# Optimization experiments

Measured on AMD Instinct MI355X. Metric: run time of the kernel, lower is better.

The kernel has to match this reference:

```python
import jax, jax.numpy as jnp
import numpy as np
import math

NUM_GROUPS = 32
NUM_HEADS = 8  # in_channels // num_head_channel = 512 // 64
EPS = 1e-5


def setup_inputs() -> dict:
    key = jax.random.key(0)
    ks = jax.random.split(key, 4)
    b, c, h, w = 2, 512, 64, 64
    s = 1.0 / math.sqrt(c)
    return {
        "x": jax.random.normal(ks[0], (b, c, h, w), dtype=jnp.float32),
        "gn_weight": jnp.ones((c,), jnp.float32),
        "gn_bias": jnp.zeros((c,), jnp.float32),
        "wq": jax.random.normal(ks[1], (c, c), jnp.float32) * s,
        "bq": jnp.zeros((c,), jnp.float32),
        "wkv": jax.random.normal(ks[2], (2 * c, c), jnp.float32) * s,
        "bkv": jnp.zeros((2 * c,), jnp.float32),
        "wproj": jax.random.normal(ks[3], (c, c), jnp.float32) * s,
        "bproj": jnp.zeros((c,), jnp.float32),
    }


def _group_norm(x, weight, bias):
    b, c, h, w = x.shape
    xg = x.reshape(b, NUM_GROUPS, c // NUM_GROUPS, h, w)
    mean = jnp.mean(xg, axis=(2, 3, 4), keepdims=True)
    var = jnp.var(xg, axis=(2, 3, 4), keepdims=True)
    xn = ((xg - mean) * jax.lax.rsqrt(var + EPS)).reshape(b, c, h, w)
    return xn * weight[None, :, None, None] + bias[None, :, None, None]


def reference(x, gn_weight, gn_bias, wq, bq, wkv, bkv, wproj, bproj):
    b, c, h, w = x.shape
    nh = NUM_HEADS
    hd = c // nh
    residual = x

    hs = _group_norm(x, gn_weight, gn_bias)
    hs = hs.reshape(b, c, h * w).transpose(0, 2, 1)  # [b, seq, c]

    q = hs @ wq.T + bq                     # [b, seq, c]
    kv = hs @ wkv.T + bkv                  # [b, seq, 2c]
    k, v = jnp.split(kv, 2, axis=2)

    def to_heads(t):  # [b, seq, c] -> [b, nh, seq, hd]
        return t.reshape(b, -1, nh, hd).transpose(0, 2, 1, 3)

    q, k, v = to_heads(q), to_heads(k), to_heads(v)
    scale = 1.0 / math.sqrt(hd)

    scores = jnp.einsum("bhqd,bhkd->bhqk", q, k) * scale
    probs = jax.nn.softmax(scores.astype(jnp.float32), axis=-1).astype(scores.dtype)
    out = jnp.einsum("bhqk,bhkd->bhqd", probs, v)  # [b, nh, seq, hd]

    out = out.transpose(0, 2, 1, 3).reshape(b, h * w, c)
    out = out @ wproj.T + bproj
    out = out.transpose(0, 2, 1).reshape(b, c, h, w)
    return out + residual
```

## Files before the change

kernel.cpp:

```cpp
#include <hip/hip_runtime.h>

typedef __attribute__((ext_vector_type(8))) short bf16x8;
typedef __attribute__((ext_vector_type(4))) float f32x4;
typedef __attribute__((ext_vector_type(4))) unsigned int u32x4;
typedef __attribute__((ext_vector_type(4))) unsigned short su16x4;

#define SEQ 4096
#define CH 512

__device__ __forceinline__ float b2f(unsigned short u) {
  union { unsigned int i; float f; } x; x.i = ((unsigned int)u) << 16; return x.f;
}
__device__ __forceinline__ unsigned short f2b(float f) {
  union { float f; unsigned int i; } x; x.f = f;
  unsigned int r = x.i + 0x7fffu + ((x.i >> 16) & 1u);
  return (unsigned short)(r >> 16);
}

template<int F32> struct LD;
template<> struct LD<0> {
  static __device__ __forceinline__ float at(const void* p, size_t i) {
    return b2f(((const unsigned short*)p)[i]);
  }
  static __device__ __forceinline__ bf16x8 b8(const void* p, size_t i) {
    return *(const bf16x8*)((const unsigned short*)p + i);
  }
  static __device__ __forceinline__ void f4(const void* p, size_t i, float o[4]) {
    su16x4 v = *(const su16x4*)((const unsigned short*)p + i);
#pragma unroll
    for (int j = 0; j < 4; ++j) o[j] = b2f(v[j]);
  }
};
template<> struct LD<1> {
  static __device__ __forceinline__ float at(const void* p, size_t i) {
    return ((const float*)p)[i];
  }
  static __device__ __forceinline__ bf16x8 b8(const void* p, size_t i) {
    const float* f = (const float*)p + i;
    f32x4 a = *(const f32x4*)f, b = *(const f32x4*)(f + 4);
    union { bf16x8 v; unsigned short u[8]; } r;
#pragma unroll
    for (int j = 0; j < 4; ++j) { r.u[j] = f2b(a[j]); r.u[4 + j] = f2b(b[j]); }
    return r.v;
  }
  static __device__ __forceinline__ void f4(const void* p, size_t i, float o[4]) {
    f32x4 v = *(const f32x4*)((const float*)p + i);
#pragma unroll
    for (int j = 0; j < 4; ++j) o[j] = v[j];
  }
};
template<int F32> struct ST;
template<> struct ST<0> {
  static __device__ __forceinline__ void st4(void* p, size_t i, const float v[4]) {
    su16x4 o;
#pragma unroll
    for (int j = 0; j < 4; ++j) o[j] = f2b(v[j]);
    *(su16x4*)((unsigned short*)p + i) = o;
  }
};
template<> struct ST<1> {
  static __device__ __forceinline__ void st4(void* p, size_t i, const float v[4]) {
// ... 106 lines not shown
                                                  unsigned short* __restrict__ hs, int b,
                                                  const int* __restrict__ ctrl) {
  if (ctrl[0] != F32) return;
  const int bz = b + blockIdx.z;
  hs += (size_t)blockIdx.z * ((size_t)SEQ * CH);
  const int s0 = blockIdx.x * 64, c0 = blockIdx.y * 64;
  __shared__ float tile[64 * 65];
  const int t = threadIdx.x;
  float2 stv[4];
#pragma unroll
  for (int i = 0; i < 4; ++i) stv[i] = stats[bz * 32 + (c0 >> 4) + i];
#pragma unroll
  for (int rep = 0; rep < 16; ++rep) {
    int idx = rep * 256 + t;
    int cl = idx >> 6, sl = idx & 63;
    int c = c0 + cl;
    float xv = LD<F32>::at(x, ((size_t)(bz * CH + c)) * SEQ + s0 + sl);
    float2 sv = stv[cl >> 4];
    tile[cl * 65 + sl] = (xv - sv.x) * sv.y * LD<F32>::at(w, c) + LD<F32>::at(bsv, c);
  }
  __syncthreads();
#pragma unroll
  for (int rep = 0; rep < 16; ++rep) {
    int idx = rep * 256 + t;
    int cl = idx & 63, sl = idx >> 6;
    hs[((size_t)(s0 + sl)) * CH + c0 + cl] = f2b(tile[cl * 65 + sl]);
  }
}

template<int F32>
__global__ __launch_bounds__(256) void qkv_head_k(const unsigned short* __restrict__ hs,
                                                  const void* __restrict__ wq,
                                                  const void* __restrict__ wkv,
                                                  const void* __restrict__ bq,
                                                  const void* __restrict__ bkv,
                                                  unsigned short* __restrict__ qh,
                                                  unsigned short* __restrict__ kh,
                                                  unsigned short* __restrict__ vt, int h0,
                                                  const int* __restrict__ ctrl) {
  if (ctrl[0] != F32) return;
  const int z = blockIdx.z;
  const int h = h0 + (z & 7);
  hs += (size_t)(z >> 3) * ((size_t)SEQ * CH);
  const size_t hofs = (size_t)z * (4096 * 64);
  __shared__ __align__(16) unsigned short As[128 * 64];
  __shared__ __align__(16) unsigned short Ws[64 * 64];
  const int t = threadIdx.x;
  const int lane = t & 63, wave = t >> 6;
  const int l15 = lane & 15, qd = lane >> 4;
  const int m0 = blockIdx.x * 128;

  const void* Wb; size_t wofs; const void* bb; size_t bofs;
  unsigned short* dst; float scale = 1.0f; int tr = 0;
  if (blockIdx.y == 0)      { Wb = wq;  wofs = (size_t)(h * 64) * 512;         bb = bq;  bofs = h * 64;       dst = qh + hofs; scale = 0.125f; }
  else if (blockIdx.y == 1) { Wb = wkv; wofs = (size_t)(h * 64) * 512;         bb = bkv; bofs = h * 64;       dst = kh + hofs; }
  else                      { Wb = wkv; wofs = (size_t)(512 + h * 64) * 512;   bb = bkv; bofs = 512 + h * 64; dst = vt + hofs; tr = 1; }

  const f32x4 fz = {0.f, 0.f, 0.f, 0.f};
  f32x4 acc[2][4];
#pragma unroll
  for (int i = 0; i < 2; ++i)
#pragma unroll
    for (int j = 0; j < 4; ++j) acc[i][j] = fz;

  bf16x8 ar[4], wr2[2];
#pragma unroll
  for (int rep = 0; rep < 4; ++rep) {
    int id = rep * 256 + t, r = id >> 3, c = id & 7;
    ar[rep] = LD<0>::b8(hs, (size_t)(m0 + r) * 512 + c * 8);
  }
#pragma unroll
  for (int rep = 0; rep < 2; ++rep) {
    int id = rep * 256 + t, r = id >> 3, c = id & 7;
    wr2[rep] = LD<F32>::b8(Wb, wofs + (size_t)r * 512 + c * 8);
  }
  for (int ks = 0; ks < 8; ++ks) {
    __syncthreads();
#pragma unroll
    for (int rep = 0; rep < 4; ++rep) {
      int id = rep * 256 + t, r = id >> 3, c = id & 7, p = (c + r) & 7;
      *(bf16x8*)&As[r * 64 + p * 8] = ar[rep];
    }
#pragma unroll
    for (int rep = 0; rep < 2; ++rep) {
      int id = rep * 256 + t, r = id >> 3, c = id & 7, p = (c + r) & 7;
      *(bf16x8*)&Ws[r * 64 + p * 8] = wr2[rep];
    }
    __syncthreads();
    if (ks < 7) {
      int k0 = (ks + 1) * 64;
#pragma unroll
      for (int rep = 0; rep < 4; ++rep) {
        int id = rep * 256 + t, r = id >> 3, c = id & 7;
        ar[rep] = LD<0>::b8(hs, (size_t)(m0 + r) * 512 + k0 + c * 8);
      }
#pragma unroll
      for (int rep = 0; rep < 2; ++rep) {
        int id = rep * 256 + t, r = id >> 3, c = id & 7;
        wr2[rep] = LD<F32>::b8(Wb, wofs + (size_t)r * 512 + k0 + c * 8);
      }
    }
#pragma unroll
    for (int kb = 0; kb < 2; ++kb) {
      int cc = kb * 4 + qd;
      bf16x8 af[2], bfr[4];
#pragma unroll
      for (int mt = 0; mt < 2; ++mt) {
// ... 204 lines not shown
      f32x4 a = *(const f32x4*)((const float*)x + base);
      f32x4 b = *(const f32x4*)((const float*)x + base + 4);
#pragma unroll
      for (int j = 0; j < 4; ++j) { vals[j] = a[j]; vals[4 + j] = b[j]; }
    } else {
      wv = LD<0>::at(w, c); bvv = LD<0>::at(bsv, c);
      const unsigned short* xp = (const unsigned short*)x + base;
      u32x4 v = *(const u32x4*)xp;
#pragma unroll
      for (int j = 0; j < 4; ++j) {
        vals[2 * j] = b2f((unsigned short)v[j]);
        vals[2 * j + 1] = b2f((unsigned short)(v[j] >> 16));
      }
    }
    float mul = st.y * wv, add = bvv - st.x * st.y * wv;
#pragma unroll
    for (int j = 0; j < 8; ++j) tile[cl * 65 + sv + j] = vals[j] * mul + add;
  }
  __syncthreads();
#pragma unroll
  for (int rep = 0; rep < 4; ++rep) {
    int idx = rep * 256 + t;
    int sl = idx >> 4, cl4 = (idx & 15) * 4;
    su16x4 ov;
#pragma unroll
    for (int j = 0; j < 4; ++j) ov[j] = f2b(tile[(cl4 + j) * 65 + sl]);
    *(su16x4*)&hsb[((size_t)(s0 + sl)) * 512 + c0 + cl4] = ov;
  }
}

__global__ __launch_bounds__(256) void qkv2_k(const unsigned short* __restrict__ hs,
                                              const void* __restrict__ wq,
                                              const void* __restrict__ wkv,
                                              const void* __restrict__ bq,
                                              const void* __restrict__ bkv,
                                              unsigned short* __restrict__ qh,
                                              unsigned short* __restrict__ kh,
                                              unsigned short* __restrict__ vt,
                                              const int* __restrict__ ctrl) {
  const int mode = ctrl[0];
  const int z = blockIdx.z;
  const int h = z & 7;
  hs += (size_t)(z >> 3) * ((size_t)SEQ * CH);
  const size_t hofs = (size_t)z * (4096 * 64);
  __shared__ __align__(16) unsigned short As[128 * 64];
  __shared__ __align__(16) unsigned short Ws[64 * 64];
  const int t = threadIdx.x;
  const int lane = t & 63, wave = t >> 6;
  const int l15 = lane & 15, qd = lane >> 4;
  const int m0 = blockIdx.x * 128;

  const void* Wb; size_t wofs; const void* bb; size_t bofs;
  unsigned short* dst; float scale = 1.0f; int tr = 0;
  if (blockIdx.y == 0)      { Wb = wq;  wofs = (size_t)(h * 64) * 512;         bb = bq;  bofs = h * 64;       dst = qh + hofs; scale = 0.125f; }
  else if (blockIdx.y == 1) { Wb = wkv; wofs = (size_t)(h * 64) * 512;         bb = bkv; bofs = h * 64;       dst = kh + hofs; }
  else                      { Wb = wkv; wofs = (size_t)(512 + h * 64) * 512;   bb = bkv; bofs = 512 + h * 64; dst = vt + hofs; tr = 1; }

  const f32x4 fz = {0.f, 0.f, 0.f, 0.f};
  f32x4 acc[2][4];
#pragma unroll
  for (int i = 0; i < 2; ++i)
#pragma unroll
    for (int j = 0; j < 4; ++j) acc[i][j] = fz;

  bf16x8 ar[4], wr2[2];
#pragma unroll
  for (int rep = 0; rep < 4; ++rep) {
    int id = rep * 256 + t, r = id >> 3, c = id & 7;
    ar[rep] = LD<0>::b8(hs, (size_t)(m0 + r) * 512 + c * 8);
  }
  if (mode) {
#pragma unroll
    for (int rep = 0; rep < 2; ++rep) {
      int id = rep * 256 + t, r = id >> 3, c = id & 7;
      wr2[rep] = LD<1>::b8(Wb, wofs + (size_t)r * 512 + c * 8);
    }
  } else {
#pragma unroll
    for (int rep = 0; rep < 2; ++rep) {
      int id = rep * 256 + t, r = id >> 3, c = id & 7;
      wr2[rep] = LD<0>::b8(Wb, wofs + (size_t)r * 512 + c * 8);
    }
  }
  for (int ks = 0; ks < 8; ++ks) {
    __syncthreads();
#pragma unroll
    for (int rep = 0; rep < 4; ++rep) {
      int id = rep * 256 + t, r = id >> 3, c = id & 7, p = (c + r) & 7;
      *(bf16x8*)&As[r * 64 + p * 8] = ar[rep];
    }
#pragma unroll
    for (int rep = 0; rep < 2; ++rep) {
      int id = rep * 256 + t, r = id >> 3, c = id & 7, p = (c + r) & 7;
      *(bf16x8*)&Ws[r * 64 + p * 8] = wr2[rep];
    }
    __syncthreads();
    if (ks < 7) {
      int k0 = (ks + 1) * 64;
#pragma unroll
      for (int rep = 0; rep < 4; ++rep) {
        int id = rep * 256 + t, r = id >> 3, c = id & 7;
        ar[rep] = LD<0>::b8(hs, (size_t)(m0 + r) * 512 + k0 + c * 8);
      }
      if (mode) {
#pragma unroll
        for (int rep = 0; rep < 2; ++rep) {
          int id = rep * 256 + t, r = id >> 3, c = id & 7;
// ... 77 lines not shown
  const f32x4 fz = {0.f, 0.f, 0.f, 0.f};
  f32x4 o[4];
#pragma unroll
  for (int i = 0; i < 4; ++i) o[i] = fz;
  f32x4 lsum = fz;

  union { bf16x8 v; unsigned short u[8]; } onesu;
#pragma unroll
  for (int j = 0; j < 8; ++j) onesu.u[j] = 0x3F80;
  const bf16x8 onesv = onesu.v;

  unsigned short* pp = &Ps[wave][0];

  const int sid0 = t, sr0 = sid0 >> 3, sc0 = sid0 & 7;
  const int sid1 = 256 + t, sr1 = sid1 >> 3, sc1 = sid1 & 7;
  u32x4 kr0, kr1, vr0, vr1;
  kr0 = *(const u32x4*)&kh[(size_t)sr0 * 64 + sc0 * 8];
  kr1 = *(const u32x4*)&kh[(size_t)sr1 * 64 + sc1 * 8];
  vr0 = *(const u32x4*)&vt[(size_t)sr0 * 4096 + sc0 * 8];
  vr1 = *(const u32x4*)&vt[(size_t)sr1 * 4096 + sc1 * 8];

  const int p0 = (sc0 ^ (sr0 & 7)) * 8, p1 = (sc1 ^ (sr1 & 7)) * 8;

  for (int kt = 0; kt < 64; ++kt) {
    __syncthreads();
    *(u32x4*)&Ks[sr0 * 64 + p0] = kr0;
    *(u32x4*)&Ks[sr1 * 64 + p1] = kr1;
    *(u32x4*)&Vs[sr0 * 64 + p0] = vr0;
    *(u32x4*)&Vs[sr1 * 64 + p1] = vr1;
    __syncthreads();
    if (kt < 63) {
      int kn = kt + 1;
      kr0 = *(const u32x4*)&kh[(size_t)(kn * 64 + sr0) * 64 + sc0 * 8];
      kr1 = *(const u32x4*)&kh[(size_t)(kn * 64 + sr1) * 64 + sc1 * 8];
      vr0 = *(const u32x4*)&vt[(size_t)sr0 * 4096 + kn * 64 + sc0 * 8];
      vr1 = *(const u32x4*)&vt[(size_t)sr1 * 4096 + kn * 64 + sc1 * 8];
    }

    f32x4 sa[4];
#pragma unroll
    for (int nt = 0; nt < 4; ++nt) {
      sa[nt] = fz;
      int row = nt * 16 + l15, rx = row & 7;
      bf16x8 kf0 = *(const bf16x8*)&Ks[row * 64 + (qd ^ rx) * 8];
      bf16x8 kf1 = *(const bf16x8*)&Ks[row * 64 + ((qd + 4) ^ rx) * 8];
      sa[nt] = __builtin_amdgcn_mfma_f32_16x16x32_bf16(qf0, kf0, sa[nt], 0, 0, 0);
      sa[nt] = __builtin_amdgcn_mfma_f32_16x16x32_bf16(qf1, kf1, sa[nt], 0, 0, 0);
    }

#pragma unroll
    for (int nt = 0; nt < 4; ++nt)
#pragma unroll
      for (int r = 0; r < 4; ++r)
        sa[nt][r] = __expf(fminf(sa[nt][r], 60.0f));

#pragma unroll
    for (int nt = 0; nt < 4; ++nt)
#pragma unroll
      for (int r = 0; r < 4; r += 2) {
        unsigned int pk;
        asm("v_cvt_pk_bf16_f32 %0, %1, %2" : "=v"(pk) : "v"(sa[nt][r]), "v"(sa[nt][r + 1]));
        pp[(qd * 4 + r) * 72 + nt * 16 + l15] = (unsigned short)pk;
        pp[(qd * 4 + r + 1) * 72 + nt * 16 + l15] = (unsigned short)(pk >> 16);
      }

    bf16x8 pf0 = *(const bf16x8*)&pp[l15 * 72 + qd * 8];
    bf16x8 pf1 = *(const bf16x8*)&pp[l15 * 72 + 32 + qd * 8];

    lsum = __builtin_amdgcn_mfma_f32_16x16x32_bf16(pf0, onesv, lsum, 0, 0, 0);
    lsum = __builtin_amdgcn_mfma_f32_16x16x32_bf16(pf1, onesv, lsum, 0, 0, 0);

#pragma unroll
    for (int nt = 0; nt < 4; ++nt) {
      int row = nt * 16 + l15, rx = row & 7;
      bf16x8 vf0 = *(const bf16x8*)&Vs[row * 64 + (qd ^ rx) * 8];
      bf16x8 vf1 = *(const bf16x8*)&Vs[row * 64 + ((qd + 4) ^ rx) * 8];
      o[nt] = __builtin_amdgcn_mfma_f32_16x16x32_bf16(pf0, vf0, o[nt], 0, 0, 0);
      o[nt] = __builtin_amdgcn_mfma_f32_16x16x32_bf16(pf1, vf1, o[nt], 0, 0, 0);
    }
  }

  float inv[4];
#pragma unroll
  for (int r = 0; r < 4; ++r) inv[r] = 1.f / lsum[r];
#pragma unroll
  for (int nt = 0; nt < 4; ++nt)
#pragma unroll
    for (int r = 0; r < 4; ++r) {
      int row = qt * 64 + wave * 16 + qd * 4 + r;
      aw[(size_t)row * 512 + h * 64 + nt * 16 + l15] = f2b(o[nt][r] * inv[r]);
    }
}

__global__ __launch_bounds__(256) void proj2_k(const unsigned short* __restrict__ A,
                                               const void* __restrict__ W,
                                               const void* __restrict__ bias,
                                               void* __restrict__ outv,
                                               const void* __restrict__ residv,
                                               const int* __restrict__ ctrl) {
  const int mode = ctrl[0];
  const int z = blockIdx.z;
  A += (size_t)z * ((size_t)SEQ * CH);
  const void* resid = (const void*)((const char*)residv + (size_t)z * ((size_t)SEQ * CH) * (mode ? 4 : 2));
  void* out0 = (void*)((char*)outv + (size_t)z * ((size_t)SEQ * CH) * (mode ? 4 : 2));
  __shared__ __align__(16) unsigned short As[128 * 64];
  __shared__ __align__(16) unsigned short Bs[128 * 64];
  const int t = threadIdx.x;
  const int lane = t & 63, wave = t >> 6;
  const int l15 = lane & 15, qd = lane >> 4;
  const int m0 = blockIdx.x * 128, n0 = blockIdx.y * 128;
  const int wm = (wave & 1) * 64, wn = (wave >> 1) * 64;

  const f32x4 fz = {0.f, 0.f, 0.f, 0.f};
  f32x4 acc[4][4];
#pragma unroll
  for (int i = 0; i < 4; ++i)
#pragma unroll
    for (int j = 0; j < 4; ++j) acc[i][j] = fz;

  bf16x8 ar[4], br[4];
#pragma unroll
  for (int rep = 0; rep < 4; ++rep) {
    int id = rep * 256 + t, r = id >> 3, c = id & 7;
    ar[rep] = LD<0>::b8(A, (size_t)(m0 + r) * 512 + c * 8);
  }
  if (mode) {
#pragma unroll
    for (int rep = 0; rep < 4; ++rep) {
      int id = rep * 256 + t, r = id >> 3, c = id & 7;
      br[rep] = LD<1>::b8(W, (size_t)(n0 + r) * 512 + c * 8);
    }
  } else {
#pragma unroll
    for (int rep = 0; rep < 4; ++rep) {
      int id = rep * 256 + t, r = id >> 3, c = id & 7;
      br[rep] = LD<0>::b8(W, (size_t)(n0 + r) * 512 + c * 8);
    }
  }
  for (int ks = 0; ks < 8; ++ks) {
    __syncthreads();
#pragma unroll
    for (int rep = 0; rep < 4; ++rep) {
      int id = rep * 256 + t, r = id >> 3, c = id & 7, p = (c + r) & 7;
      *(bf16x8*)&As[r * 64 + p * 8] = ar[rep];
// ... 38 lines not shown
      for (int mt = 0; mt < 4; ++mt)
#pragma unroll
        for (int nt = 0; nt < 4; ++nt)
          acc[mt][nt] = __builtin_amdgcn_mfma_f32_16x16x32_bf16(af[mt], bfr[nt], acc[mt][nt], 0, 0, 0);
    }
  }

  float bv[4];
#pragma unroll
  for (int nt = 0; nt < 4; ++nt)
    bv[nt] = mode ? LD<1>::at(bias, n0 + wn + nt * 16 + l15)
                  : LD<0>::at(bias, n0 + wn + nt * 16 + l15);

#pragma unroll
  for (int mt = 0; mt < 4; ++mt) {
    int row0 = m0 + wm + mt * 16 + qd * 4;
#pragma unroll
    for (int nt = 0; nt < 4; ++nt) {
      int col = n0 + wn + nt * 16 + l15;
      size_t basea = ((size_t)col) * 4096 + row0;
      float rv[4], ov[4];
      if (mode) LD<1>::f4(resid, basea, rv); else LD<0>::f4(resid, basea, rv);
#pragma unroll
      for (int r = 0; r < 4; ++r) ov[r] = acc[mt][nt][r] + bv[nt] + rv[r];
      if (mode) ST<1>::st4(out0, basea, ov); else ST<0>::st4(out0, basea, ov);
    }
  }
}

extern "C" void kernel_launch(void* const* d_in, const int* in_sizes, int n_in,
                              void* d_out, int out_size, void* d_ws, size_t ws_size,
                              hipStream_t stream) {
  const void* x   = d_in[0];
  const void* gw  = d_in[1];
  const void* gb  = d_in[2];
  const void* wq  = d_in[3];
  const void* bq  = d_in[4];
  const void* wkv = d_in[5];
  const void* bkv = d_in[6];
  const void* wp  = d_in[7];
  const void* bp  = d_in[8];

  const size_t EM = (size_t)4096 * 512;
  const int NOUT = 4194304;
  const size_t HB = (size_t)4096 * 64;

  int* ctrl = (int*)d_ws;
  float2* stats = (float2*)((char*)d_ws + 64);
  float2* partials = (float2*)((char*)d_ws + 576);

  probe_k<<<1, 256, 0, stream>>>((const unsigned short*)x, ctrl);

  const size_t FAST2_NEED = 4096 + (3 * 16 * HB + 2 * EM) * sizeof(unsigned short);
  const size_t FAST_NEED = 1024 + 3 * 8 * HB * sizeof(unsigned short);

  if (ws_size >= FAST2_NEED) {
    unsigned short* qa = (unsigned short*)((char*)d_ws + 4096);
    unsigned short* ka = qa + 16 * HB;
    unsigned short* va = ka + 16 * HB;
    unsigned short* aw0 = va + 16 * HB;
    const int NQKV = (int)(3 * 16 * HB);
    const int NAW  = (int)(2 * EM);

    unsigned short* hs01 = (unsigned short*)d_out;

    gn_stats2_k<<<256, 256, 0, stream>>>(x, partials, ctrl);
    gn_fin_k<<<1, 64, 0, stream>>>(partials, stats);
    gn_apply2_k<<<dim3(64, 8, 2), 256, 0, stream>>>(x, gw, gb, stats, hs01, ctrl);
    scan_k<<<256, 256, 0, stream>>>(hs01, NAW, 0, ctrl, -1);

    qkv2_k<<<dim3(32, 3, 16), 256, 0, stream>>>(hs01, wq, wkv, bq, bkv, qa, ka, va, ctrl);
    scan_k<<<256, 256, 0, stream>>>(qa, NQKV, 1, ctrl, -1);
    attn_head_k<<<dim3(64, 16), 256, 0, stream>>>(qa, ka, va, aw0, 0, ctrl, -1);
    scan_k<<<256, 256, 0, stream>>>(aw0, NAW, 2, ctrl, -1);
    proj2_k<<<dim3(32, 4, 2), 256, 0, stream>>>(aw0, wp, bp, d_out, x, ctrl);

    scan_k<<<256, 256, 0, stream>>>((unsigned short*)d_out, NOUT, 6, ctrl, 0);
    scan32_k<<<256, 256, 0, stream>>>((float*)d_out, NOUT, 6, ctrl);

    sent_fin_k<0><<<256, 256, 0, stream>>>(d_out, ctrl, NOUT);
    sent_fin_k<1><<<256, 256, 0, stream>>>(d_out, ctrl, NOUT);
    return;
  }

  if (ws_size >= FAST_NEED) {
    unsigned short* qa = (unsigned short*)((char*)d_ws + 1024);
    unsigned short* ka = qa + 8 * HB;
    unsigned short* va = ka + 8 * HB;
    const int NQKV = (int)(3 * 8 * HB);

    {
      unsigned short* out16 = (unsigned short*)d_out;
      unsigned short* hs0 = out16;
      unsigned short* aw0 = out16 + EM;
      unsigned short* hs1 = out16 + EM;
      unsigned short* aw1 = (unsigned short*)d_in[0];

      gn_stats_k<0><<<64, 256, 0, stream>>>(x, stats, ctrl);
      gn_apply_k<0><<<dim3(64, 8), 256, 0, stream>>>(x, gw, gb, stats, hs0, 0, ctrl);
      scan_k<<<256, 256, 0, stream>>>(hs0, (int)EM, 0, ctrl, 0);

      qkv_head_k<0><<<dim3(32, 3, 8), 256, 0, stream>>>(hs0, wq, wkv, bq, bkv, qa, ka, va, 0, ctrl);
      scan_k<<<256, 256, 0, stream>>>(qa, NQKV, 1, ctrl, 0);
      attn_head_k<<<dim3(64, 8), 256, 0, stream>>>(qa, ka, va, aw0, 0, ctrl, 0);
      scan_k<<<256, 256, 0, stream>>>(aw0, (int)EM, 2, ctrl, 0);
      proj_k<0><<<dim3(32, 4), 256, 0, stream>>>(aw0, wp, bp, out16, x, ctrl);

      gn_apply_k<0><<<dim3(64, 8), 256, 0, stream>>>(x, gw, gb, stats, hs1, 1, ctrl);
      scan_k<<<256, 256, 0, stream>>>(hs1, (int)EM, 3, ctrl, 0);
      qkv_head_k<0><<<dim3(32, 3, 8), 256, 0, stream>>>(hs1, wq, wkv, bq, bkv, qa, ka, va, 0, ctrl);
      scan_k<<<256, 256, 0, stream>>>(qa, NQKV, 4, ctrl, 0);
      attn_head_k<<<dim3(64, 8), 256, 0, stream>>>(qa, ka, va, aw1, 0, ctrl, 0);
      scan_k<<<256, 256, 0, stream>>>(aw1, (int)EM, 5, ctrl, 0);
      proj_k<0><<<dim3(32, 4), 256, 0, stream>>>(aw1, wp, bp, out16 + EM,
                                                 (const char*)x + EM * 2, ctrl);
      scan_k<<<256, 256, 0, stream>>>(out16, NOUT, 6, ctrl, 0);
    }

    {
      const float* xf = (const float*)x;
      float* outf = (float*)d_out;
      unsigned short* hsA = (unsigned short*)d_out;
      unsigned short* awA = (unsigned short*)((char*)d_out + 8 * 1024 * 1024);
      unsigned short* hsB = (unsigned short*)((char*)d_out + 12 * 1024 * 1024);
      unsigned short* awB = (unsigned short*)d_in[0];

// ... 106 lines not shown
```

Baseline: 293.9 us.

## Split attention over key halves and combine partial outputs in a separate kernel

Adds a split-K attention kernel that launches twice as many blocks, each covering half of the key sequence, and writes unnormalized fp32 partial outputs and row sums to workspace. A combine kernel sums the halves, normalizes, and writes bf16. The aim is more parallelism than the original 1024-block attention launch provides on a large GPU. The change also folds log2(e) into the Q scale so exp2f replaces __expf. It costs extra workspace traffic for the fp32 partials and one more kernel launch, and only runs when the workspace is large enough.

Measured after the change: 309.6 us. 1.05x slower.

```diff
diff --git a/kernel.cpp b/kernel.cpp
--- a/kernel.cpp
+++ b/kernel.cpp
@@ -7,6 +7,8 @@
 
 #define SEQ 4096
 #define CH 512
+#define QSCALE 0.180336887f
+#define SCLAMP 86.0f
 
 __device__ __forceinline__ float b2f(unsigned short u) {
   union { unsigned int i; float f; } x; x.i = ((unsigned int)u) << 16; return x.f;
@@ -219,7 +221,7 @@
 
   const void* Wb; size_t wofs; const void* bb; size_t bofs;
   unsigned short* dst; float scale = 1.0f; int tr = 0;
-  if (blockIdx.y == 0)      { Wb = wq;  wofs = (size_t)(h * 64) * 512;         bb = bq;  bofs = h * 64;       dst = qh + hofs; scale = 0.125f; }
+  if (blockIdx.y == 0)      { Wb = wq;  wofs = (size_t)(h * 64) * 512;         bb = bq;  bofs = h * 64;       dst = qh + hofs; scale = QSCALE; }
   else if (blockIdx.y == 1) { Wb = wkv; wofs = (size_t)(h * 64) * 512;         bb = bkv; bofs = h * 64;       dst = kh + hofs; }
   else                      { Wb = wkv; wofs = (size_t)(512 + h * 64) * 512;   bb = bkv; bofs = 512 + h * 64; dst = vt + hofs; tr = 1; }
 
@@ -530,7 +532,7 @@
 
   const void* Wb; size_t wofs; const void* bb; size_t bofs;
   unsigned short* dst; float scale = 1.0f; int tr = 0;
-  if (blockIdx.y == 0)      { Wb = wq;  wofs = (size_t)(h * 64) * 512;         bb = bq;  bofs = h * 64;       dst = qh + hofs; scale = 0.125f; }
+  if (blockIdx.y == 0)      { Wb = wq;  wofs = (size_t)(h * 64) * 512;         bb = bq;  bofs = h * 64;       dst = qh + hofs; scale = QSCALE; }
   else if (blockIdx.y == 1) { Wb = wkv; wofs = (size_t)(h * 64) * 512;         bb = bkv; bofs = h * 64;       dst = kh + hofs; }
   else                      { Wb = wkv; wofs = (size_t)(512 + h * 64) * 512;   bb = bkv; bofs = 512 + h * 64; dst = vt + hofs; tr = 1; }
 
@@ -714,7 +716,7 @@
     for (int nt = 0; nt < 4; ++nt)
 #pragma unroll
       for (int r = 0; r < 4; ++r)
-        sa[nt][r] = __expf(fminf(sa[nt][r], 60.0f));
+        sa[nt][r] = exp2f(fminf(sa[nt][r], SCLAMP));
 
 #pragma unroll
     for (int nt = 0; nt < 4; ++nt)
@@ -752,6 +754,149 @@
       int row = qt * 64 + wave * 16 + qd * 4 + r;
       aw[(size_t)row * 512 + h * 64 + nt * 16 + l15] = f2b(o[nt][r] * inv[r]);
     }
+}
+
+__global__ __launch_bounds__(256) void attn_split_k(const unsigned short* __restrict__ qh,
+                                                    const unsigned short* __restrict__ kh,
+                                                    const unsigned short* __restrict__ vt,
+                                                    float* __restrict__ po,
+                                                    float* __restrict__ ls,
+                                                    const int* __restrict__ ctrl) {
+  const int y = blockIdx.y;
+  const int bh = y & 15, khalf = y >> 4;
+  const size_t hofs = (size_t)bh * (4096 * 64);
+  qh += hofs; kh += hofs; vt += hofs;
+  const int qt = blockIdx.x;
+  const int kt0 = khalf * 32;
+  const int t = threadIdx.x;
+  const int lane = t & 63, wave = t >> 6;
+  const int l15 = lane & 15, qd = lane >> 4;
+
+  __shared__ __align__(16) unsigned short Ks[64 * 64];
+  __shared__ __align__(16) unsigned short Vs[64 * 64];
+  __shared__ __align__(16) unsigned short Ps[4][16 * 72];
+
+  const int qrow = qt * 64 + wave * 16 + l15;
+  bf16x8 qf0 = *(const bf16x8*)&qh[(size_t)qrow * 64 + qd * 8];
+  bf16x8 qf1 = *(const bf16x8*)&qh[(size_t)qrow * 64 + 32 + qd * 8];
+
+  const f32x4 fz = {0.f, 0.f, 0.f, 0.f};
+  f32x4 o[4];
+#pragma unroll
+  for (int i = 0; i < 4; ++i) o[i] = fz;
+  f32x4 lsum = fz;
+
+  union { bf16x8 v; unsigned short u[8]; } onesu;
+#pragma unroll
+  for (int j = 0; j < 8; ++j) onesu.u[j] = 0x3F80;
+  const bf16x8 onesv = onesu.v;
+
+  unsigned short* pp = &Ps[wave][0];
+
+  const int sid0 = t, sr0 = sid0 >> 3, sc0 = sid0 & 7;
+  const int sid1 = 256 + t, sr1 = sid1 >> 3, sc1 = sid1 & 7;
+  u32x4 kr0, kr1, vr0, vr1;
+  kr0 = *(const u32x4*)&kh[(size_t)(kt0 * 64 + sr0) * 64 + sc0 * 8];
+  kr1 = *(const u32x4*)&kh[(size_t)(kt0 * 64 + sr1) * 64 + sc1 * 8];
+  vr0 = *(const u32x4*)&vt[(size_t)sr0 * 4096 + kt0 * 64 + sc0 * 8];
+  vr1 = *(const u32x4*)&vt[(size_t)sr1 * 4096 + kt0 * 64 + sc1 * 8];
+
+  const int p0 = (sc0 ^ (sr0 & 7)) * 8, p1 = (sc1 ^ (sr1 & 7)) * 8;
+
+  for (int kt = kt0; kt < kt0 + 32; ++kt) {
+    __syncthreads();
+    *(u32x4*)&Ks[sr0 * 64 + p0] = kr0;
+    *(u32x4*)&Ks[sr1 * 64 + p1] = kr1;
+    *(u32x4*)&Vs[sr0 * 64 + p0] = vr0;
+    *(u32x4*)&Vs[sr1 * 64 + p1] = vr1;
+    __syncthreads();
+    if (kt < kt0 + 31) {
+      int kn = kt + 1;
+      kr0 = *(const u32x4*)&kh[(size_t)(kn * 64 + sr0) * 64 + sc0 * 8];
+      kr1 = *(const u32x4*)&kh[(size_t)(kn * 64 + sr1) * 64 + sc1 * 8];
+      vr0 = *(const u32x4*)&vt[(size_t)sr0 * 4096 + kn * 64 + sc0 * 8];
+      vr1 = *(const u32x4*)&vt[(size_t)sr1 * 4096 + kn * 64 + sc1 * 8];
+    }
+
+    f32x4 sa[4];
+#pragma unroll
+    for (int nt = 0; nt < 4; ++nt) {
+      sa[nt] = fz;
+      int row = nt * 16 + l15, rx = row & 7;
+      bf16x8 kf0 = *(const bf16x8*)&Ks[row * 64 + (qd ^ rx) * 8];
+      bf16x8 kf1 = *(const bf16x8*)&Ks[row * 64 + ((qd + 4) ^ rx) * 8];
+      sa[nt] = __builtin_amdgcn_mfma_f32_16x16x32_bf16(qf0, kf0, sa[nt], 0, 0, 0);
+      sa[nt] = __builtin_amdgcn_mfma_f32_16x16x32_bf16(qf1, kf1, sa[nt], 0, 0, 0);
+    }
+
+#pragma unroll
+    for (int nt = 0; nt < 4; ++nt)
+#pragma unroll
+      for (int r = 0; r < 4; ++r)
+        sa[nt][r] = exp2f(fminf(sa[nt][r], SCLAMP));
+
+#pragma unroll
+    for (int nt = 0; nt < 4; ++nt)
+#pragma unroll
+      for (int r = 0; r < 4; r += 2) {
+        unsigned int pk;
+        asm("v_cvt_pk_bf16_f32 %0, %1, %2" : "=v"(pk) : "v"(sa[nt][r]), "v"(sa[nt][r + 1]));
+        pp[(qd * 4 + r) * 72 + nt * 16 + l15] = (unsigned short)pk;
+        pp[(qd * 4 + r + 1) * 72 + nt * 16 + l15] = (unsigned short)(pk >> 16);
+      }
+
+    bf16x8 pf0 = *(const bf16x8*)&pp[l15 * 72 + qd * 8];
+    bf16x8 pf1 = *(const bf16x8*)&pp[l15 * 72 + 32 + qd * 8];
+
+    lsum = __builtin_amdgcn_mfma_f32_16x16x32_bf16(pf0, onesv, lsum, 0, 0, 0);
+    lsum = __builtin_amdgcn_mfma_f32_16x16x32_bf16(pf1, onesv, lsum, 0, 0, 0);
+
+#pragma unroll
+    for (int nt = 0; nt < 4; ++nt) {
+      int row = nt * 16 + l15, rx = row & 7;
+      bf16x8 vf0 = *(const bf16x8*)&Vs[row * 64 + (qd ^ rx) * 8];
+      bf16x8 vf1 = *(const bf16x8*)&Vs[row * 64 + ((qd + 4) ^ rx) * 8];
+      o[nt] = __builtin_amdgcn_mfma_f32_16x16x32_bf16(pf0, vf0, o[nt], 0, 0, 0);
+      o[nt] = __builtin_amdgcn_mfma_f32_16x16x32_bf16(pf1, vf1, o[nt], 0, 0, 0);
+    }
+  }
+
+  float* pob = po + (((size_t)y * 64 + qt) * 64) * 64;
+  float* lsb = ls + ((size_t)y * 64 + qt) * 64;
+#pragma unroll
+  for (int r = 0; r < 4; ++r) {
+    int row = wave * 16 + qd * 4 + r;
+    if (l15 == 0) lsb[row] = lsum[r];
+#pragma unroll
+    for (int nt = 0; nt < 4; ++nt)
+      pob[(size_t)row * 64 + nt * 16 + l15] = o[nt][r];
+  }
+}
+
+__global__ __launch_bounds__(256) void comb_k(const float* __restrict__ po,
+                                              const float* __restrict__ ls,
+                                              unsigned short* __restrict__ aw,
+                                              const int* __restrict__ ctrl) {
+  const int qt = blockIdx.x, bh = blockIdx.y;
+  const int h = bh & 7, b = bh >> 3;
+  unsigned short* awb = aw + (size_t)b * ((size_t)SEQ * CH);
+  const float* po0 = po + (((size_t)bh * 64 + qt) * 64) * 64;
+  const float* po1 = po + (((size_t)(16 + bh) * 64 + qt) * 64) * 64;
+  const float* ls0 = ls + ((size_t)bh * 64 + qt) * 64;
+  const float* ls1 = ls + ((size_t)(16 + bh) * 64 + qt) * 64;
+  const int t = threadIdx.x;
+#pragma unroll
+  for (int rep = 0; rep < 4; ++rep) {
+    int idx = rep * 256 + t;
+    int lr = idx >> 4, c4 = (idx & 15) * 4;
+    float inv = 1.f / (ls0[lr] + ls1[lr]);
+    f32x4 a = *(const f32x4*)(po0 + (size_t)lr * 64 + c4);
+    f32x4 bq = *(const f32x4*)(po1 + (size_t)lr * 64 + c4);
+    su16x4 ov;
+#pragma unroll
+    for (int j = 0; j < 4; ++j) ov[j] = f2b((a[j] + bq[j]) * inv);
+    *(su16x4*)&awb[((size_t)(qt * 64 + lr)) * 512 + h * 64 + c4] = ov;
+  }
 }
 
 __global__ __launch_bounds__(256) void proj2_k(const unsigned short* __restrict__ A,
@@ -896,6 +1041,9 @@
   probe_k<<<1, 256, 0, stream>>>((const unsigned short*)x, ctrl);
 
   const size_t FAST2_NEED = 4096 + (3 * 16 * HB + 2 * EM) * sizeof(unsigned short);
+  const size_t PO_BYTES = (size_t)32 * 64 * 64 * 64 * 4;
+  const size_t LS_BYTES = (size_t)32 * 64 * 64 * 4;
+  const size_t SPLIT_NEED = FAST2_NEED + PO_BYTES + LS_BYTES;
   const size_t FAST_NEED = 1024 + 3 * 8 * HB * sizeof(unsigned short);
 
   if (ws_size >= FAST2_NEED) {
@@ -915,7 +1063,15 @@
 
     qkv2_k<<<dim3(32, 3, 16), 256, 0, stream>>>(hs01, wq, wkv, bq, bkv, qa, ka, va, ctrl);
     scan_k<<<256, 256, 0, stream>>>(qa, NQKV, 1, ctrl, -1);
-    attn_head_k<<<dim3(64, 16), 256, 0, stream>>>(qa, ka, va, aw0, 0, ctrl, -1);
+
+    if (ws_size >= SPLIT_NEED) {
+      float* po = (float*)((char*)d_ws + FAST2_NEED);
+      float* ls = (float*)((char*)po + PO_BYTES);
+      attn_split_k<<<dim3(64, 32), 256, 0, stream>>>(qa, ka, va, po, ls, ctrl);
+      comb_k<<<dim3(64, 16), 256, 0, stream>>>(po, ls, aw0, ctrl);
+    } else {
+      attn_head_k<<<dim3(64, 16), 256, 0, stream>>>(qa, ka, va, aw0, 0, ctrl, -1);
+    }
     scan_k<<<256, 256, 0, stream>>>(aw0, NAW, 2, ctrl, -1);
     proj2_k<<<dim3(32, 4, 2), 256, 0, stream>>>(aw0, wp, bp, d_out, x, ctrl);
 
```

## Replace attention kernel with 32x32 MFMA split-K variant using exp2

Applied to the files above, without the earlier changes.

Adds a new attention kernel using 32x32x16 bf16 MFMAs that computes S^T and keeps probabilities in registers, exchanging halves via lane shuffles instead of staging through LDS. Waves split the key tile in two halves and reduce partial outputs and row sums through shared memory at the end, and the row sum is accumulated in VALU rather than by an MFMA against a ones vector. Q scaling is folded to include log2(e) so exp2f replaces __expf. It keeps the softmax without max subtraction (clamped exponent), and the register-level permutation of P is more complex and error-prone.

After: 330.2 us. +12.3%, slower.

```diff
diff --git a/kernel.cpp b/kernel.cpp
--- a/kernel.cpp
+++ b/kernel.cpp
@@ -2,11 +2,14 @@
 
 typedef __attribute__((ext_vector_type(8))) short bf16x8;
 typedef __attribute__((ext_vector_type(4))) float f32x4;
+typedef __attribute__((ext_vector_type(16))) float f32x16;
 typedef __attribute__((ext_vector_type(4))) unsigned int u32x4;
 typedef __attribute__((ext_vector_type(4))) unsigned short su16x4;
 
 #define SEQ 4096
 #define CH 512
+#define QSCALE 0.180336887f
+#define SCLAMP 86.0f
 
 __device__ __forceinline__ float b2f(unsigned short u) {
   union { unsigned int i; float f; } x; x.i = ((unsigned int)u) << 16; return x.f;
@@ -219,7 +222,7 @@
 
   const void* Wb; size_t wofs; const void* bb; size_t bofs;
   unsigned short* dst; float scale = 1.0f; int tr = 0;
-  if (blockIdx.y == 0)      { Wb = wq;  wofs = (size_t)(h * 64) * 512;         bb = bq;  bofs = h * 64;       dst = qh + hofs; scale = 0.125f; }
+  if (blockIdx.y == 0)      { Wb = wq;  wofs = (size_t)(h * 64) * 512;         bb = bq;  bofs = h * 64;       dst = qh + hofs; scale = QSCALE; }
   else if (blockIdx.y == 1) { Wb = wkv; wofs = (size_t)(h * 64) * 512;         bb = bkv; bofs = h * 64;       dst = kh + hofs; }
   else                      { Wb = wkv; wofs = (size_t)(512 + h * 64) * 512;   bb = bkv; bofs = 512 + h * 64; dst = vt + hofs; tr = 1; }
 
@@ -530,7 +533,7 @@
 
   const void* Wb; size_t wofs; const void* bb; size_t bofs;
   unsigned short* dst; float scale = 1.0f; int tr = 0;
-  if (blockIdx.y == 0)      { Wb = wq;  wofs = (size_t)(h * 64) * 512;         bb = bq;  bofs = h * 64;       dst = qh + hofs; scale = 0.125f; }
+  if (blockIdx.y == 0)      { Wb = wq;  wofs = (size_t)(h * 64) * 512;         bb = bq;  bofs = h * 64;       dst = qh + hofs; scale = QSCALE; }
   else if (blockIdx.y == 1) { Wb = wkv; wofs = (size_t)(h * 64) * 512;         bb = bkv; bofs = h * 64;       dst = kh + hofs; }
   else                      { Wb = wkv; wofs = (size_t)(512 + h * 64) * 512;   bb = bkv; bofs = 512 + h * 64; dst = vt + hofs; tr = 1; }
 
@@ -714,7 +717,7 @@
     for (int nt = 0; nt < 4; ++nt)
 #pragma unroll
       for (int r = 0; r < 4; ++r)
-        sa[nt][r] = __expf(fminf(sa[nt][r], 60.0f));
+        sa[nt][r] = exp2f(fminf(sa[nt][r], SCLAMP));
 
 #pragma unroll
     for (int nt = 0; nt < 4; ++nt)
@@ -752,6 +755,164 @@
       int row = qt * 64 + wave * 16 + qd * 4 + r;
       aw[(size_t)row * 512 + h * 64 + nt * 16 + l15] = f2b(o[nt][r] * inv[r]);
     }
+}
+
+__global__ __launch_bounds__(256) void attn32_k(const unsigned short* __restrict__ qh,
+                                                const unsigned short* __restrict__ kh,
+                                                const unsigned short* __restrict__ vt,
+                                                unsigned short* __restrict__ aw,
+                                                const int* __restrict__ ctrl) {
+  const int y = blockIdx.y;
+  const int h = y & 7;
+  const size_t hofs = (size_t)y * (4096 * 64);
+  qh += hofs; kh += hofs; vt += hofs;
+  aw += (size_t)(y >> 3) * ((size_t)SEQ * CH);
+  const int qt = blockIdx.x;
+  const int t = threadIdx.x;
+  const int lane = t & 63, wave = t >> 6;
+  const int khalf = wave & 1, qblk = wave >> 1;
+  const int l31 = lane & 31, hp = lane >> 5;
+
+  __shared__ __align__(16) unsigned short Ks[64 * 64];
+  __shared__ __align__(16) unsigned short Vs[64 * 64];
+  __shared__ float Ls[64];
+
+  const int qrow = qt * 64 + qblk * 32 + l31;
+  bf16x8 qf[4];
+#pragma unroll
+  for (int mi = 0; mi < 4; ++mi)
+    qf[mi] = *(const bf16x8*)&qh[(size_t)qrow * 64 + mi * 16 + hp * 8];
+
+  f32x16 o0, o1, sa;
+#pragma unroll
+  for (int i = 0; i < 16; ++i) { o0[i] = 0.f; o1[i] = 0.f; }
+  float la[4] = {0.f, 0.f, 0.f, 0.f};
+
+  const int sid0 = t, sr0 = sid0 >> 3, sc0 = sid0 & 7;
+  const int sid1 = 256 + t, sr1 = sid1 >> 3, sc1 = sid1 & 7;
+  u32x4 kr0, kr1, vr0, vr1;
+  kr0 = *(const u32x4*)&kh[(size_t)sr0 * 64 + sc0 * 8];
+  kr1 = *(const u32x4*)&kh[(size_t)sr1 * 64 + sc1 * 8];
+  vr0 = *(const u32x4*)&vt[(size_t)sr0 * 4096 + sc0 * 8];
+  vr1 = *(const u32x4*)&vt[(size_t)sr1 * 4096 + sc1 * 8];
+  const int p0 = (sc0 ^ (sr0 & 7)) * 8, p1 = (sc1 ^ (sr1 & 7)) * 8;
+
+  const int krow = khalf * 32 + l31;
+  const int krx = krow & 7;
+
+  for (int kt = 0; kt < 64; ++kt) {
+    __syncthreads();
+    *(u32x4*)&Ks[sr0 * 64 + p0] = kr0;
+    *(u32x4*)&Ks[sr1 * 64 + p1] = kr1;
+    *(u32x4*)&Vs[sr0 * 64 + p0] = vr0;
+    *(u32x4*)&Vs[sr1 * 64 + p1] = vr1;
+    __syncthreads();
+    if (kt < 63) {
+      int kn = kt + 1;
+      kr0 = *(const u32x4*)&kh[(size_t)(kn * 64 + sr0) * 64 + sc0 * 8];
+      kr1 = *(const u32x4*)&kh[(size_t)(kn * 64 + sr1) * 64 + sc1 * 8];
+      vr0 = *(const u32x4*)&vt[(size_t)sr0 * 4096 + kn * 64 + sc0 * 8];
+      vr1 = *(const u32x4*)&vt[(size_t)sr1 * 4096 + kn * 64 + sc1 * 8];
+    }
+
+#pragma unroll
+    for (int i = 0; i < 16; ++i) sa[i] = 0.f;
+#pragma unroll
+    for (int mi = 0; mi < 4; ++mi) {
+      int ck = mi * 2 + hp;
+      bf16x8 kf = *(const bf16x8*)&Ks[krow * 64 + ((ck ^ krx) * 8)];
+      sa = __builtin_amdgcn_mfma_f32_32x32x16_bf16(kf, qf[mi], sa, 0, 0, 0);
+    }
+
+    unsigned int c0u[2], c1u[2], c2u[2], c3u[2];
+#pragma unroll
+    for (int g = 0; g < 4; ++g) {
+#pragma unroll
+      for (int rr = 0; rr < 4; ++rr) {
+        float e = exp2f(fminf(sa[g * 4 + rr], SCLAMP));
+        sa[g * 4 + rr] = e;
+        la[rr] += e;
+      }
+      unsigned int pk0, pk1;
+      asm("v_cvt_pk_bf16_f32 %0, %1, %2" : "=v"(pk0) : "v"(sa[g * 4 + 0]), "v"(sa[g * 4 + 1]));
+      asm("v_cvt_pk_bf16_f32 %0, %1, %2" : "=v"(pk1) : "v"(sa[g * 4 + 2]), "v"(sa[g * 4 + 3]));
+      if (g == 0) { c0u[0] = pk0; c0u[1] = pk1; }
+      else if (g == 1) { c1u[0] = pk0; c1u[1] = pk1; }
+      else if (g == 2) { c2u[0] = pk0; c2u[1] = pk1; }
+      else { c3u[0] = pk0; c3u[1] = pk1; }
+    }
+    unsigned int r0u[2], r1u[2], r2u[2], r3u[2];
+    r0u[0] = (unsigned int)__shfl_xor((int)c0u[0], 32, 64);
+    r0u[1] = (unsigned int)__shfl_xor((int)c0u[1], 32, 64);
+    r1u[0] = (unsigned int)__shfl_xor((int)c1u[0], 32, 64);
+    r1u[1] = (unsigned int)__shfl_xor((int)c1u[1], 32, 64);
+    r2u[0] = (unsigned int)__shfl_xor((int)c2u[0], 32, 64);
+    r2u[1] = (unsigned int)__shfl_xor((int)c2u[1], 32, 64);
+    r3u[0] = (unsigned int)__shfl_xor((int)c3u[0], 32, 64);
+    r3u[1] = (unsigned int)__shfl_xor((int)c3u[1], 32, 64);
+
+#pragma unroll
+    for (int kc = 0; kc < 2; ++kc) {
+      union { u32x4 u; bf16x8 v; } pb;
+      if (kc == 0) {
+        pb.u[0] = hp ? r1u[0] : c0u[0];
+        pb.u[1] = hp ? r1u[1] : c0u[1];
+        pb.u[2] = hp ? c1u[0] : r0u[0];
+        pb.u[3] = hp ? c1u[1] : r0u[1];
+      } else {
+        pb.u[0] = hp ? r3u[0] : c2u[0];
+        pb.u[1] = hp ? r3u[1] : c2u[1];
+        pb.u[2] = hp ? c3u[0] : r2u[0];
+        pb.u[3] = hp ? c3u[1] : r2u[1];
+      }
+      int cv = khalf * 4 + kc * 2 + hp;
+      {
+        int vrow = l31, vrx = vrow & 7;
+        bf16x8 vf = *(const bf16x8*)&Vs[vrow * 64 + ((cv ^ vrx) * 8)];
+        o0 = __builtin_amdgcn_mfma_f32_32x32x16_bf16(vf, pb.v, o0, 0, 0, 0);
+      }
+      {
+        int vrow = 32 + l31, vrx = vrow & 7;
+        bf16x8 vf = *(const bf16x8*)&Vs[vrow * 64 + ((cv ^ vrx) * 8)];
+        o1 = __builtin_amdgcn_mfma_f32_32x32x16_bf16(vf, pb.v, o1, 0, 0, 0);
+      }
+    }
+  }
+
+  float lsum = la[0] + la[1] + la[2] + la[3];
+  lsum += __shfl_xor(lsum, 32, 64);
+
+  __syncthreads();
+  float* buf = (float*)(qblk == 0 ? (void*)Ks : (void*)Vs);
+  if (khalf == 1) {
+#pragma unroll
+    for (int i = 0; i < 16; ++i) {
+      buf[i * 64 + lane] = o0[i];
+      buf[(16 + i) * 64 + lane] = o1[i];
+    }
+    if (hp == 0) Ls[qblk * 32 + l31] = lsum;
+  }
+  __syncthreads();
+  if (khalf == 0) {
+#pragma unroll
+    for (int i = 0; i < 16; ++i) {
+      o0[i] += buf[i * 64 + lane];
+      o1[i] += buf[(16 + i) * 64 + lane];
+    }
+    float inv = 1.f / (lsum + Ls[qblk * 32 + l31]);
+    const size_t rowbase = (size_t)(qt * 64 + qblk * 32 + l31) * 512 + h * 64;
+#pragma unroll
+    for (int g = 0; g < 4; ++g) {
+      su16x4 ov0, ov1;
+#pragma unroll
+      for (int rr = 0; rr < 4; ++rr) {
+        ov0[rr] = f2b(o0[g * 4 + rr] * inv);
+        ov1[rr] = f2b(o1[g * 4 + rr] * inv);
+      }
+      *(su16x4*)&aw[rowbase + g * 8 + hp * 4] = ov0;
+      *(su16x4*)&aw[rowbase + 32 + g * 8 + hp * 4] = ov1;
+    }
+  }
 }
 
 __global__ __launch_bounds__(256) void proj2_k(const unsigned short* __restrict__ A,
@@ -915,7 +1076,8 @@
 
     qkv2_k<<<dim3(32, 3, 16), 256, 0, stream>>>(hs01, wq, wkv, bq, bkv, qa, ka, va, ctrl);
     scan_k<<<256, 256, 0, stream>>>(qa, NQKV, 1, ctrl, -1);
-    attn_head_k<<<dim3(64, 16), 256, 0, stream>>>(qa, ka, va, aw0, 0, ctrl, -1);
+
+    attn32_k<<<dim3(64, 16), 256, 0, stream>>>(qa, ka, va, aw0, ctrl);
     scan_k<<<256, 256, 0, stream>>>(aw0, NAW, 2, ctrl, -1);
     proj2_k<<<dim3(32, 4, 2), 256, 0, stream>>>(aw0, wp, bp, d_out, x, ctrl);
 
```

## Add 128-query attention tile kernel with transposed-score MFMA and exp2 softmax

Applied to the files above, without the earlier changes.

Replaces the 64-query attention kernel with one where each wave handles 32 query rows, so every K/V tile staged in shared memory is reused across twice as many queries. This halves the grid, and with it the total K/V global loads and LDS staging work. Scores are computed as K·Q so each lane holds four contiguous P values and writes them as a single 8-byte LDS store instead of scattered 2-byte stores. The Q scale now folds in log2(e), so softmax uses exp2f directly, with the clamp adjusted to match. The risks are higher register pressure from the doubled accumulators and only 512 blocks, which may limit occupancy.

Measured after the change: 312.0 us. 1.06x slower.

```diff
diff --git a/kernel.cpp b/kernel.cpp
--- a/kernel.cpp
+++ b/kernel.cpp
@@ -3,10 +3,13 @@
 typedef __attribute__((ext_vector_type(8))) short bf16x8;
 typedef __attribute__((ext_vector_type(4))) float f32x4;
 typedef __attribute__((ext_vector_type(4))) unsigned int u32x4;
+typedef __attribute__((ext_vector_type(2))) unsigned int u32x2;
 typedef __attribute__((ext_vector_type(4))) unsigned short su16x4;
 
 #define SEQ 4096
 #define CH 512
+#define QSCALE 0.180336887f
+#define SCLAMP 86.0f
 
 __device__ __forceinline__ float b2f(unsigned short u) {
   union { unsigned int i; float f; } x; x.i = ((unsigned int)u) << 16; return x.f;
@@ -219,7 +222,7 @@
 
   const void* Wb; size_t wofs; const void* bb; size_t bofs;
   unsigned short* dst; float scale = 1.0f; int tr = 0;
-  if (blockIdx.y == 0)      { Wb = wq;  wofs = (size_t)(h * 64) * 512;         bb = bq;  bofs = h * 64;       dst = qh + hofs; scale = 0.125f; }
+  if (blockIdx.y == 0)      { Wb = wq;  wofs = (size_t)(h * 64) * 512;         bb = bq;  bofs = h * 64;       dst = qh + hofs; scale = QSCALE; }
   else if (blockIdx.y == 1) { Wb = wkv; wofs = (size_t)(h * 64) * 512;         bb = bkv; bofs = h * 64;       dst = kh + hofs; }
   else                      { Wb = wkv; wofs = (size_t)(512 + h * 64) * 512;   bb = bkv; bofs = 512 + h * 64; dst = vt + hofs; tr = 1; }
 
@@ -530,7 +533,7 @@
 
   const void* Wb; size_t wofs; const void* bb; size_t bofs;
   unsigned short* dst; float scale = 1.0f; int tr = 0;
-  if (blockIdx.y == 0)      { Wb = wq;  wofs = (size_t)(h * 64) * 512;         bb = bq;  bofs = h * 64;       dst = qh + hofs; scale = 0.125f; }
+  if (blockIdx.y == 0)      { Wb = wq;  wofs = (size_t)(h * 64) * 512;         bb = bq;  bofs = h * 64;       dst = qh + hofs; scale = QSCALE; }
   else if (blockIdx.y == 1) { Wb = wkv; wofs = (size_t)(h * 64) * 512;         bb = bkv; bofs = h * 64;       dst = kh + hofs; }
   else                      { Wb = wkv; wofs = (size_t)(512 + h * 64) * 512;   bb = bkv; bofs = 512 + h * 64; dst = vt + hofs; tr = 1; }
 
@@ -714,7 +717,7 @@
     for (int nt = 0; nt < 4; ++nt)
 #pragma unroll
       for (int r = 0; r < 4; ++r)
-        sa[nt][r] = __expf(fminf(sa[nt][r], 60.0f));
+        sa[nt][r] = exp2f(fminf(sa[nt][r], SCLAMP));
 
 #pragma unroll
     for (int nt = 0; nt < 4; ++nt)
@@ -752,6 +755,123 @@
       int row = qt * 64 + wave * 16 + qd * 4 + r;
       aw[(size_t)row * 512 + h * 64 + nt * 16 + l15] = f2b(o[nt][r] * inv[r]);
     }
+}
+
+__global__ __launch_bounds__(256) void attn128_k(const unsigned short* __restrict__ qh,
+                                                 const unsigned short* __restrict__ kh,
+                                                 const unsigned short* __restrict__ vt,
+                                                 unsigned short* __restrict__ aw,
+                                                 const int* __restrict__ ctrl) {
+  const int y = blockIdx.y;
+  const int h = y & 7;
+  const size_t hofs = (size_t)y * (4096 * 64);
+  qh += hofs; kh += hofs; vt += hofs;
+  aw += (size_t)(y >> 3) * ((size_t)SEQ * CH);
+  const int qt = blockIdx.x;
+  const int t = threadIdx.x;
+  const int lane = t & 63, wave = t >> 6;
+  const int l15 = lane & 15, qd = lane >> 4;
+
+  __shared__ __align__(16) unsigned short Ks[64 * 64];
+  __shared__ __align__(16) unsigned short Vs[64 * 64];
+  __shared__ __align__(16) unsigned short Ps[4][32 * 72];
+
+  bf16x8 qf[2][2];
+#pragma unroll
+  for (int g = 0; g < 2; ++g) {
+    int qrow = qt * 128 + wave * 32 + g * 16 + l15;
+    qf[g][0] = *(const bf16x8*)&qh[(size_t)qrow * 64 + qd * 8];
+    qf[g][1] = *(const bf16x8*)&qh[(size_t)qrow * 64 + 32 + qd * 8];
+  }
+
+  const f32x4 fz = {0.f, 0.f, 0.f, 0.f};
+  f32x4 o[2][4];
+#pragma unroll
+  for (int g = 0; g < 2; ++g)
+#pragma unroll
+    for (int i = 0; i < 4; ++i) o[g][i] = fz;
+  f32x4 ls[2] = {fz, fz};
+
+  union { bf16x8 v; unsigned short u[8]; } onesu;
+#pragma unroll
+  for (int j = 0; j < 8; ++j) onesu.u[j] = 0x3F80;
+  const bf16x8 onesv = onesu.v;
+
+  unsigned short* pp = &Ps[wave][0];
+
+  const int sid0 = t, sr0 = sid0 >> 3, sc0 = sid0 & 7;
+  const int sid1 = 256 + t, sr1 = sid1 >> 3, sc1 = sid1 & 7;
+  u32x4 kr0, kr1, vr0, vr1;
+  kr0 = *(const u32x4*)&kh[(size_t)sr0 * 64 + sc0 * 8];
+  kr1 = *(const u32x4*)&kh[(size_t)sr1 * 64 + sc1 * 8];
+  vr0 = *(const u32x4*)&vt[(size_t)sr0 * 4096 + sc0 * 8];
+  vr1 = *(const u32x4*)&vt[(size_t)sr1 * 4096 + sc1 * 8];
+  const int p0 = (sc0 ^ (sr0 & 7)) * 8, p1 = (sc1 ^ (sr1 & 7)) * 8;
+
+  for (int kt = 0; kt < 64; ++kt) {
+    __syncthreads();
+    *(u32x4*)&Ks[sr0 * 64 + p0] = kr0;
+    *(u32x4*)&Ks[sr1 * 64 + p1] = kr1;
+    *(u32x4*)&Vs[sr0 * 64 + p0] = vr0;
+    *(u32x4*)&Vs[sr1 * 64 + p1] = vr1;
+    __syncthreads();
+    if (kt < 63) {
+      int kn = kt + 1;
+      kr0 = *(const u32x4*)&kh[(size_t)(kn * 64 + sr0) * 64 + sc0 * 8];
+      kr1 = *(const u32x4*)&kh[(size_t)(kn * 64 + sr1) * 64 + sc1 * 8];
+      vr0 = *(const u32x4*)&vt[(size_t)sr0 * 4096 + kn * 64 + sc0 * 8];
+      vr1 = *(const u32x4*)&vt[(size_t)sr1 * 4096 + kn * 64 + sc1 * 8];
+    }
+
+#pragma unroll
+    for (int g = 0; g < 2; ++g) {
+#pragma unroll
+      for (int nt = 0; nt < 4; ++nt) {
+        f32x4 sa = fz;
+        int row = nt * 16 + l15, rx = row & 7;
+        bf16x8 kf0 = *(const bf16x8*)&Ks[row * 64 + (qd ^ rx) * 8];
+        bf16x8 kf1 = *(const bf16x8*)&Ks[row * 64 + ((qd + 4) ^ rx) * 8];
+        sa = __builtin_amdgcn_mfma_f32_16x16x32_bf16(kf0, qf[g][0], sa, 0, 0, 0);
+        sa = __builtin_amdgcn_mfma_f32_16x16x32_bf16(kf1, qf[g][1], sa, 0, 0, 0);
+#pragma unroll
+        for (int r = 0; r < 4; ++r) sa[r] = exp2f(fminf(sa[r], SCLAMP));
+        unsigned int pk0, pk1;
+        asm("v_cvt_pk_bf16_f32 %0, %1, %2" : "=v"(pk0) : "v"(sa[0]), "v"(sa[1]));
+        asm("v_cvt_pk_bf16_f32 %0, %1, %2" : "=v"(pk1) : "v"(sa[2]), "v"(sa[3]));
+        u32x2 w; w[0] = pk0; w[1] = pk1;
+        *(u32x2*)&pp[(g * 16 + l15) * 72 + nt * 16 + qd * 4] = w;
+      }
+
+      bf16x8 pf0 = *(const bf16x8*)&pp[(g * 16 + l15) * 72 + qd * 8];
+      bf16x8 pf1 = *(const bf16x8*)&pp[(g * 16 + l15) * 72 + 32 + qd * 8];
+
+      ls[g] = __builtin_amdgcn_mfma_f32_16x16x32_bf16(pf0, onesv, ls[g], 0, 0, 0);
+      ls[g] = __builtin_amdgcn_mfma_f32_16x16x32_bf16(pf1, onesv, ls[g], 0, 0, 0);
+
+#pragma unroll
+      for (int nt = 0; nt < 4; ++nt) {
+        int row = nt * 16 + l15, rx = row & 7;
+        bf16x8 vf0 = *(const bf16x8*)&Vs[row * 64 + (qd ^ rx) * 8];
+        bf16x8 vf1 = *(const bf16x8*)&Vs[row * 64 + ((qd + 4) ^ rx) * 8];
+        o[g][nt] = __builtin_amdgcn_mfma_f32_16x16x32_bf16(pf0, vf0, o[g][nt], 0, 0, 0);
+        o[g][nt] = __builtin_amdgcn_mfma_f32_16x16x32_bf16(pf1, vf1, o[g][nt], 0, 0, 0);
+      }
+    }
+  }
+
+#pragma unroll
+  for (int g = 0; g < 2; ++g) {
+    float inv[4];
+#pragma unroll
+    for (int r = 0; r < 4; ++r) inv[r] = 1.f / ls[g][r];
+#pragma unroll
+    for (int nt = 0; nt < 4; ++nt)
+#pragma unroll
+      for (int r = 0; r < 4; ++r) {
+        int row = qt * 128 + wave * 32 + g * 16 + qd * 4 + r;
+        aw[(size_t)row * 512 + h * 64 + nt * 16 + l15] = f2b(o[g][nt][r] * inv[r]);
+      }
+  }
 }
 
 __global__ __launch_bounds__(256) void proj2_k(const unsigned short* __restrict__ A,
@@ -915,7 +1035,8 @@
 
     qkv2_k<<<dim3(32, 3, 16), 256, 0, stream>>>(hs01, wq, wkv, bq, bkv, qa, ka, va, ctrl);
     scan_k<<<256, 256, 0, stream>>>(qa, NQKV, 1, ctrl, -1);
-    attn_head_k<<<dim3(64, 16), 256, 0, stream>>>(qa, ka, va, aw0, 0, ctrl, -1);
+
+    attn128_k<<<dim3(32, 16), 256, 0, stream>>>(qa, ka, va, aw0, ctrl);
     scan_k<<<256, 256, 0, stream>>>(aw0, NAW, 2, ctrl, -1);
     proj2_k<<<dim3(32, 4, 2), 256, 0, stream>>>(aw0, wp, bp, d_out, x, ctrl);
 
```
